# Kernel tuning notes

Measured on AMD Instinct MI355X. Metric: run time of the kernel, lower is better.

The kernel has to match this reference:

```python
import jax, jax.numpy as jnp
import numpy as np
import math

B, L, D = 2, 2048, 1024
H = 16
DH = D // H  # 64
XPOS_SCALE_BASE = 512.0
THETA = 10000.0


def setup_inputs() -> dict:
    key = jax.random.key(0)
    ks = jax.random.split(key, 9)
    s = 0.02  # keep logits in a sane range like trained weights
    return {
        "x": jax.random.normal(ks[0], (B, L, D), dtype=jnp.float32),
        "Wq": jax.random.normal(ks[1], (D, D), dtype=jnp.float32) * s,
        "bq": jax.random.normal(ks[2], (D,), dtype=jnp.float32) * s,
        "Wk": jax.random.normal(ks[3], (D, D), dtype=jnp.float32) * s,
        "bk": jax.random.normal(ks[4], (D,), dtype=jnp.float32) * s,
        "Wv": jax.random.normal(ks[5], (D, D), dtype=jnp.float32) * s,
        "bv": jax.random.normal(ks[6], (D,), dtype=jnp.float32) * s,
        "Wo": jax.random.normal(ks[7], (D, D), dtype=jnp.float32) * s,
        "bo": jax.random.normal(ks[8], (D,), dtype=jnp.float32) * s,
    }


def _rotate_half(t):
    # pairwise interleaved rotation, as in rotary_embedding_torch
    t1 = t[..., 0::2]
    t2 = t[..., 1::2]
    return jnp.stack([-t2, t1], axis=-1).reshape(t.shape)


def _xpos_rotate(q, k):
    # q, k: [B, H, L, DH]; xPos rotary embedding (use_xpos=True)
    seq = q.shape[2]
    half = jnp.arange(0, DH, 2, dtype=jnp.float32)
    inv_freq = 1.0 / (THETA ** (half / DH))            # [DH/2]
    t = jnp.arange(seq, dtype=jnp.float32)             # [L]
    freqs = t[:, None] * inv_freq[None, :]             # [L, DH/2]
    freqs = jnp.repeat(freqs, 2, axis=-1)              # [L, DH] interleaved
    # xPos length-extrapolatable scale
    scale_vec = (half + 0.4 * DH) / (1.4 * DH)         # [DH/2]
    power = (t - seq // 2) / XPOS_SCALE_BASE           # [L]
    scale = scale_vec[None, :] ** power[:, None]       # [L, DH/2]
    scale = jnp.repeat(scale, 2, axis=-1)              # [L, DH]
    cos = jnp.cos(freqs)
    sin = jnp.sin(freqs)
    q_out = q * (cos * scale) + _rotate_half(q) * (sin * scale)
    k_out = k * (cos / scale) + _rotate_half(k) * (sin / scale)
    return q_out, k_out


def reference(x, Wq, bq, Wk, bk, Wv, bv, Wo, bo):
    b, l, d = x.shape
    # projections; note source swaps names: v_mat <- k-proj, k_mat <- v-proj
    q = (x @ Wq.T + bq).reshape(b, l, H, DH).transpose(0, 2, 1, 3)  # [b,h,l,dh]
    v = (x @ Wk.T + bk).reshape(b, l, H, DH).transpose(0, 2, 1, 3)
    k = (x @ Wv.T + bv).reshape(b, l, H, DH).transpose(0, 2, 1, 3)
    q, k = _xpos_rotate(q, k)
    # source divides by sqrt(Dh * num_heads) == sqrt(dim)
    scores = jnp.einsum("bhqd,bhkd->bhqk", q, k) / math.sqrt(d)
    weights = jax.nn.softmax(scores, axis=-1)
    inter = jnp.einsum("bhqk,bhkd->bhqd", weights, v)
    inter = inter.transpose(0, 2, 1, 3).reshape(b, l, d)
    return inter @ Wo.T + bo
```

## Files before the change

kernel.cpp:

```cpp
#include <hip/hip_runtime.h>
#include <math.h>

#define NB 2
#define NL 2048
#define ND 1024
#define NH 16
#define NDH 64
#define NBL 4096

typedef __attribute__((ext_vector_type(4)))  float f32x4;
typedef __attribute__((ext_vector_type(16))) float f32x16;
typedef __attribute__((ext_vector_type(8)))  short s16x8;
typedef __attribute__((ext_vector_type(4)))  short s16x4;

#define LOG2E 1.44269504088896f

__device__ __forceinline__ float fexp2(float x){
#if __has_builtin(__builtin_amdgcn_exp2f)
  return __builtin_amdgcn_exp2f(x);
#else
  return exp2f(x);
#endif
}

__device__ __forceinline__ unsigned short f2bf(float f){
  unsigned int u = __float_as_uint(f);
  u += 0x7FFF + ((u >> 16) & 1);
  return (unsigned short)(u >> 16);
}

__device__ __forceinline__ unsigned int pk2bf(float lo, float hi){
  return __builtin_amdgcn_perm(__float_as_uint(hi) + 0x8000u,
                               __float_as_uint(lo) + 0x8000u, 0x07060302u);
}

__global__ void cvt_all(const float* __restrict__ x,
                        const float* __restrict__ wq, const float* __restrict__ wk,
                        const float* __restrict__ wv, const float* __restrict__ wo,
                        unsigned short* __restrict__ xb,
                        unsigned short* __restrict__ wqb, unsigned short* __restrict__ wkb,
                        unsigned short* __restrict__ wvb, unsigned short* __restrict__ wob,
                        float2* __restrict__ qtab, float2* __restrict__ ktab){
  int i = blockIdx.x * blockDim.x + threadIdx.x;
  if (i < (1<<21)){
    const float* s; unsigned short* d; int off;
    if (i < (1<<20)) { s = x; d = xb; off = i; }
    else {
      int j = i - (1<<20); int w = j >> 18; off = j & ((1<<18)-1);
      s = (w==0)?wq:(w==1)?wk:(w==2)?wv:wo;
      d = (w==0)?wqb:(w==1)?wkb:(w==2)?wvb:wob;
    }
    float4 f = reinterpret_cast<const float4*>(s)[off];
    ushort4 r; r.x=f2bf(f.x); r.y=f2bf(f.y); r.z=f2bf(f.z); r.w=f2bf(f.w);
    reinterpret_cast<ushort4*>(d)[off] = r;
  } else {
    int t = i - (1<<21);
    int l = t >> 5, k = t & 31;
    float half = 2.0f * (float)k;
    float inv_freq = 1.0f / powf(10000.0f, half / 64.0f);
    float fr = (float)l * inv_freq;
    float sv = (half + 0.4f * 64.0f) / (1.4f * 64.0f);
    float pw = ((float)l - 1024.0f) / 512.0f;
    float sc = powf(sv, pw);
    float cs = cosf(fr), sn = sinf(fr);
    qtab[t] = make_float2(cs * sc, sn * sc);
    ktab[t] = make_float2(cs / sc, sn / sc);
  }
}

__global__ __launch_bounds__(256, 4) void gemm_qkv(
    const unsigned short* __restrict__ A,
    const unsigned short* __restrict__ Wq, const float* __restrict__ bq,
    const unsigned short* __restrict__ Wk, const float* __restrict__ bk,
    const unsigned short* __restrict__ Wv, const float* __restrict__ bv,
    unsigned short* __restrict__ qb, unsigned short* __restrict__ kb,
    unsigned short* __restrict__ vtb,
    const float2* __restrict__ qtab, const float2* __restrict__ ktab)
{
  __shared__ unsigned short smem[9216];

  const int mode = blockIdx.z;
  const unsigned short* W = (mode==0) ? Wq : (mode==1) ? Wk : Wv;
  const float* bias       = (mode==0) ? bq : (mode==1) ? bk : bv;

  const int tid  = threadIdx.x;
  const int wave = tid >> 6, lane = tid & 63;
  const int m16  = lane & 15, quad = lane >> 4;
  const int mrow = (wave & 1) * 64, ncol = (wave >> 1) * 32;
  const int rA   = lane >> 2, cA = (lane & 3) * 8;
  const int row0 = blockIdx.x * 128, col0 = blockIdx.y * 64;

  f32x4 acc[4][2] = {};

  for (int k0 = 0; k0 < ND; k0 += 32){
    __syncthreads();
#pragma unroll
    for (int i3 = 0; i3 < 3; i3++){
      const int c = wave * 3 + i3;
      const unsigned short* g; unsigned short* l;
      if (c < 8){ g = A + (size_t)(row0 + c*16 + rA) * ND + k0 + cA;      l = &smem[c*512]; }
      else      { g = W + (size_t)(col0 + (c-8)*16 + rA) * ND + k0 + cA;  l = &smem[4096 + (c-8)*512]; }
      __builtin_amdgcn_global_load_lds((const __attribute__((address_space(1))) void*)g,
                                       (__attribute__((address_space(3))) void*)l, 16, 0, 0);
    }
    __syncthreads();
    s16x8 af[4], bf[2];
#pragma unroll
    for (int mt = 0; mt < 4; mt++)
      af[mt] = *reinterpret_cast<const s16x8*>(&smem[(mrow + mt*16 + m16)*32 + quad*8]);
#pragma unroll
    for (int nt = 0; nt < 2; nt++)
      bf[nt] = *reinterpret_cast<const s16x8*>(&smem[4096 + (ncol + nt*16 + m16)*32 + quad*8]);
#pragma unroll
    for (int mt = 0; mt < 4; mt++)
#pragma unroll
      for (int nt = 0; nt < 2; nt++)
        acc[mt][nt] = __builtin_amdgcn_mfma_f32_16x16x32_bf16(af[mt], bf[nt], acc[mt][nt], 0, 0, 0);
  }
  __syncthreads();

  const int b  = row0 >> 11, l0 = row0 & (NL - 1);
  const int h  = col0 >> 6;
  const int bh = b * NH + h;

  if (mode == 2){
#pragma unroll
    for (int mt = 0; mt < 4; mt++)
#pragma unroll
      for (int nt = 0; nt < 2; nt++)
#pragma unroll
        for (int r = 0; r < 4; r++){
          int lrow = mrow + mt*16 + quad*4 + r;
          int dhl  = ncol + nt*16 + m16;
          smem[lrow*72 + dhl] = f2bf(acc[mt][nt][r] + bias[col0 + dhl]);
        }
  } else {
    const float qscale = (mode == 0) ? (0.03125f * LOG2E) : 1.0f;
    const float2* tab  = (mode == 0) ? qtab : ktab;
#pragma unroll
    for (int mt = 0; mt < 4; mt++)
#pragma unroll
      for (int nt = 0; nt < 2; nt++)
#pragma unroll
        for (int r = 0; r < 4; r++){
          int lrow = mrow + mt*16 + quad*4 + r;
          int dhl  = ncol + nt*16 + m16;
          float v  = acc[mt][nt][r] + bias[col0 + dhl];
          float pv = __shfl_xor(v, 1);
          float2 t = tab[(l0 + lrow)*32 + (dhl >> 1)];
          float rh = (dhl & 1) ? pv : -pv;
          smem[lrow*72 + dhl] = f2bf((v * t.x + rh * t.y) * qscale);
        }
  }
  __syncthreads();

  if (mode == 2){
#pragma unroll
    for (int j4 = 0; j4 < 4; j4++){
      int c = tid * 4 + j4;
      int d = c >> 4, seg = (c & 15) * 8;
      unsigned short tmp[8];
#pragma unroll
      for (int jj = 0; jj < 8; jj++) tmp[jj] = smem[(seg + jj)*72 + d];
      *reinterpret_cast<uint4*>(vtb + (size_t)(bh * NDH + d) * NL + l0 + seg) =
          *reinterpret_cast<uint4*>(tmp);
    }
  } else {
    unsigned short* dst = ((mode == 0) ? qb : kb) + ((size_t)bh * NL + l0) * NDH;
#pragma unroll
    for (int j = 0; j < 4; j++){
      int idx = j*256 + tid;
      int row = idx >> 3, cg = (idx & 7) * 8;
      *reinterpret_cast<uint4*>(dst + row*NDH + cg) =
          *reinterpret_cast<const uint4*>(&smem[row*72 + cg]);
    }
  }
}

__global__ __launch_bounds__(256) void gemm_o(
    const unsigned short* __restrict__ A, const unsigned short* __restrict__ W,
    const float* __restrict__ bias, float* __restrict__ out)
{
  __shared__ unsigned short As[128][32];
  __shared__ unsigned short Bs[64][32];
  const int tid  = threadIdx.x;
  const int wave = tid >> 6, lane = tid & 63;
  const int m16  = lane & 15, quad = lane >> 4;
  const int mrow = (wave & 1) * 64, ncol = (wave >> 1) * 32;
  const int rA   = lane >> 2, cA = (lane & 3) * 8;
  const int row0 = blockIdx.x * 128, col0 = blockIdx.y * 64;

  f32x4 acc[4][2] = {};

  for (int k0 = 0; k0 < ND; k0 += 32){
    __syncthreads();
#pragma unroll
    for (int i3 = 0; i3 < 3; i3++){
      const int c = wave * 3 + i3;
      const unsigned short* g; unsigned short* l;
      if (c < 8){ g = A + (size_t)(row0 + c*16 + rA) * ND + k0 + cA;      l = &As[c*16][0]; }
      else      { g = W + (size_t)(col0 + (c-8)*16 + rA) * ND + k0 + cA;  l = &Bs[(c-8)*16][0]; }
      __builtin_amdgcn_global_load_lds((const __attribute__((address_space(1))) void*)g,
                                       (__attribute__((address_space(3))) void*)l, 16, 0, 0);
    }
    __syncthreads();
    s16x8 af[4], bf[2];
#pragma unroll
    for (int mt = 0; mt < 4; mt++) af[mt] = *reinterpret_cast<const s16x8*>(&As[mrow + mt*16 + m16][quad*8]);
#pragma unroll
    for (int nt = 0; nt < 2; nt++) bf[nt] = *reinterpret_cast<const s16x8*>(&Bs[ncol + nt*16 + m16][quad*8]);
#pragma unroll
    for (int mt = 0; mt < 4; mt++)
#pragma unroll
      for (int nt = 0; nt < 2; nt++)
        acc[mt][nt] = __builtin_amdgcn_mfma_f32_16x16x32_bf16(af[mt], bf[nt], acc[mt][nt], 0, 0, 0);
  }

#pragma unroll
  for (int mt = 0; mt < 4; mt++)
#pragma unroll
    for (int nt = 0; nt < 2; nt++)
#pragma unroll
      for (int r = 0; r < 4; r++){
        int grow = row0 + mrow + mt*16 + quad*4 + r;
        int gcol = col0 + ncol + nt*16 + m16;
        out[(size_t)grow * ND + gcol] = acc[mt][nt][r] + bias[gcol];
      }
}

__global__ __launch_bounds__(256, 2) void attn_kernel(
    const unsigned short* __restrict__ qb,
    const unsigned short* __restrict__ kb,
    const unsigned short* __restrict__ vtb,
    unsigned short* __restrict__ opart,
    float* __restrict__ lsum)
{
  __shared__ unsigned short smem[256 * 72];
  const int tid  = threadIdx.x;
  const int wave = tid >> 6, lane = tid & 63;
  const int l31  = lane & 31, g = lane >> 5;
  const int bh   = blockIdx.y;
  const int z    = blockIdx.z;
  const int q0   = blockIdx.x * 256;
  const int kbase = z * (NL / 2);
  const unsigned short* Q  = qb  + (size_t)bh * NL * NDH;
  const unsigned short* K  = kb  + (size_t)bh * NL * NDH;
  const unsigned short* Vt = vtb + (size_t)bh * NDH * NL;

  s16x8 qf[2][4];
#pragma unroll
  for (int q2 = 0; q2 < 2; q2++)
#pragma unroll
    for (int s = 0; s < 4; s++)
      qf[q2][s] = *reinterpret_cast<const s16x8*>(
          Q + (size_t)(q0 + wave*64 + q2*32 + l31) * NDH + s*16 + g*8);

  const int r0 = tid >> 3, c0 = tid & 7;
  const int r1 = r0 + 32;
  const int so0 = r0*64 + ((c0 ^ (r0 & 7)) * 8);
  const int so1 = r1*64 + ((c0 ^ (r1 & 7)) * 8);

  uint4 kreg0 = *reinterpret_cast<const uint4*>(K  + (size_t)(kbase + r0) * NDH + c0*8);
  uint4 kreg1 = *reinterpret_cast<const uint4*>(K  + (size_t)(kbase + r1) * NDH + c0*8);
  uint4 vreg0 = *reinterpret_cast<const uint4*>(Vt + (size_t)r0 * NL + kbase + c0*8);
  uint4 vreg1 = *reinterpret_cast<const uint4*>(Vt + (size_t)r1 * NL + kbase + c0*8);
  *reinterpret_cast<uint4*>(&smem[so0])         = kreg0;
  *reinterpret_cast<uint4*>(&smem[so1])         = kreg1;
  *reinterpret_cast<uint4*>(&smem[8192 + so0])  = vreg0;
  *reinterpret_cast<uint4*>(&smem[8192 + so1])  = vreg1;
  kreg0 = *reinterpret_cast<const uint4*>(K  + (size_t)(kbase + 64 + r0) * NDH + c0*8);
  kreg1 = *reinterpret_cast<const uint4*>(K  + (size_t)(kbase + 64 + r1) * NDH + c0*8);
  vreg0 = *reinterpret_cast<const uint4*>(Vt + (size_t)r0 * NL + kbase + 64 + c0*8);
  vreg1 = *reinterpret_cast<const uint4*>(Vt + (size_t)r1 * NL + kbase + 64 + c0*8);
  __syncthreads();

  float ls[2] = {0.f, 0.f};
  f32x16 ot[2][2] = {};
  const int key7 = l31 & 7;

  for (int kt = 0; kt < 16; kt++){
    const int cur = (kt & 1) * 4096;
    const int nxt = 4096 - cur;
    if (kt < 15){
      *reinterpret_cast<uint4*>(&smem[nxt + so0])        = kreg0;
      *reinterpret_cast<uint4*>(&smem[nxt + so1])        = kreg1;
      *reinterpret_cast<uint4*>(&smem[8192 + nxt + so0]) = vreg0;
      *reinterpret_cast<uint4*>(&smem[8192 + nxt + so1]) = vreg1;
    }
    if (kt < 14){
      const int k0n = kbase + (kt + 2) * 64;
      kreg0 = *reinterpret_cast<const uint4*>(K  + (size_t)(k0n + r0) * NDH + c0*8);
      kreg1 = *reinterpret_cast<const uint4*>(K  + (size_t)(k0n + r1) * NDH + c0*8);
      vreg0 = *reinterpret_cast<const uint4*>(Vt + (size_t)r0 * NL + k0n + c0*8);
      vreg1 = *reinterpret_cast<const uint4*>(Vt + (size_t)r1 * NL + k0n + c0*8);
    }

    const unsigned short* Kb = &smem[cur];
    const unsigned short* Vb = &smem[8192 + cur];

    uint2 pmat[2][8];
#pragma unroll
    for (int t = 0; t < 2; t++){
      f32x16 st0 = {}, st1 = {};
#pragma unroll
      for (int s = 0; s < 4; s++){
        const int cg = (2*s + g) ^ key7;
        s16x8 kf = *reinterpret_cast<const s16x8*>(&Kb[(t*32 + l31)*64 + cg*8]);
        st0 = __builtin_amdgcn_mfma_f32_32x32x16_bf16(kf, qf[0][s], st0, 0, 0, 0);
        st1 = __builtin_amdgcn_mfma_f32_32x32x16_bf16(kf, qf[1][s], st1, 0, 0, 0);
      }
#pragma unroll
      for (int j = 0; j < 4; j++){
        float a0 = fexp2(st0[4*j]), a1 = fexp2(st0[4*j+1]);
        float a2 = fexp2(st0[4*j+2]), a3 = fexp2(st0[4*j+3]);
        ls[0] += (a0 + a1) + (a2 + a3);
        pmat[0][t*4+j].x = pk2bf(a0, a1);
        pmat[0][t*4+j].y = pk2bf(a2, a3);
        float b0 = fexp2(st1[4*j]), b1 = fexp2(st1[4*j+1]);
        float b2 = fexp2(st1[4*j+2]), b3 = fexp2(st1[4*j+3]);
        ls[1] += (b0 + b1) + (b2 + b3);
        pmat[1][t*4+j].x = pk2bf(b0, b1);
        pmat[1][t*4+j].y = pk2bf(b2, b3);
      }
    }

#pragma unroll
    for (int mt = 0; mt < 2; mt++){
      const int dh = mt*32 + l31;
#pragma unroll
      for (int s = 0; s < 8; s++){
        const int cg = s ^ (dh & 7);
        s16x4 vf = *reinterpret_cast<const s16x4*>(&Vb[dh*64 + cg*8 + g*4]);
        ot[mt][0] = __builtin_amdgcn_mfma_f32_32x32x8bf16_1k(
            vf, *reinterpret_cast<s16x4*>(&pmat[0][s]), ot[mt][0], 0, 0, 0);
        ot[mt][1] = __builtin_amdgcn_mfma_f32_32x32x8bf16_1k(
            vf, *reinterpret_cast<s16x4*>(&pmat[1][s]), ot[mt][1], 0, 0, 0);
      }
    }
    __syncthreads();
  }

#pragma unroll
  for (int q2 = 0; q2 < 2; q2++){
    float t = ls[q2] + __shfl_xor(ls[q2], 32);
    if (g == 0)
      lsum[((size_t)z * NB * NH + bh) * NL + q0 + wave*64 + q2*32 + l31] = t;
  }

#pragma unroll
  for (int mt = 0; mt < 2; mt++)
#pragma unroll
    for (int q2 = 0; q2 < 2; q2++)
#pragma unroll
      for (int s = 0; s < 4; s++){
        uint2 pk;
        pk.x = pk2bf(ot[mt][q2][4*s], ot[mt][q2][4*s + 1]);
        pk.y = pk2bf(ot[mt][q2][4*s + 2], ot[mt][q2][4*s + 3]);
        *reinterpret_cast<uint2*>(&smem[(wave*64 + q2*32 + l31)*72 + mt*32 + s*8 + g*4]) = pk;
      }
  __syncthreads();

  const int bb = bh >> 4, h = bh & 15;
  unsigned short* od = opart + (size_t)z * NBL * ND;
#pragma unroll
  for (int j = 0; j < 8; j++){
    int idx = j*256 + tid;
    int row = idx >> 3, cg2 = (idx & 7) * 8;
    *reinterpret_cast<uint4*>(od + ((size_t)(bb*NL + q0 + row)) * ND + h*NDH + cg2) =
        *reinterpret_cast<const uint4*>(&smem[row*72 + cg2]);
  }
}

__device__ __forceinline__ unsigned int comb2(unsigned int a, unsigned int b, float inv){
  float alo = __uint_as_float(a << 16), ahi = __uint_as_float(a & 0xFFFF0000u);
  float blo = __uint_as_float(b << 16), bhi = __uint_as_float(b & 0xFFFF0000u);
  return pk2bf((alo + blo) * inv, (ahi + bhi) * inv);
}

__global__ __launch_bounds__(256) void attn_combine(
    unsigned short* __restrict__ opart, const float* __restrict__ lsum)
{
  int idx = blockIdx.x * 256 + threadIdx.x;
  int row = idx >> 7;
  int col8 = idx & 127;
  int h = col8 >> 3;
  int b = row >> 11, l = row & (NL - 1);
  int bh = b * NH + h;
  float l0 = lsum[(size_t)bh * NL + l];
  float l1 = lsum[(size_t)(NB*NH + bh) * NL + l];
  float inv = 1.0f / (l0 + l1);
  uint4 u0 = reinterpret_cast<const uint4*>(opart)[idx];
  uint4 u1 = reinterpret_cast<const uint4*>(opart + (size_t)NBL * ND)[idx];
  uint4 o;
  o.x = comb2(u0.x, u1.x, inv);
  o.y = comb2(u0.y, u1.y, inv);
  o.z = comb2(u0.z, u1.z, inv);
  o.w = comb2(u0.w, u1.w, inv);
  reinterpret_cast<uint4*>(opart)[idx] = o;
}

extern "C" void kernel_launch(void* const* d_in, const int* in_sizes, int n_in,
                              void* d_out, int out_size, void* d_ws, size_t ws_size,
                              hipStream_t stream)
{
  (void)in_sizes; (void)n_in; (void)out_size; (void)ws_size;
  const float* x  = (const float*)d_in[0];
  const float* Wq = (const float*)d_in[1];
  const float* bq = (const float*)d_in[2];
  const float* Wk = (const float*)d_in[3];
  const float* bk = (const float*)d_in[4];
  const float* Wv = (const float*)d_in[5];
  const float* bv = (const float*)d_in[6];
  const float* Wo = (const float*)d_in[7];
  const float* bo = (const float*)d_in[8];
  float* out = (float*)d_out;

  char* p = (char*)d_ws;
  unsigned short* xb    = (unsigned short*)p; p += (size_t)NBL*ND*2;
  unsigned short* wqb   = (unsigned short*)p; p += (size_t)ND*ND*2;
  unsigned short* wkb   = (unsigned short*)p; p += (size_t)ND*ND*2;
  unsigned short* wvb   = (unsigned short*)p; p += (size_t)ND*ND*2;
  unsigned short* wob   = (unsigned short*)p; p += (size_t)ND*ND*2;
  unsigned short* qbuf  = (unsigned short*)p; p += (size_t)NBL*ND*2;
  unsigned short* kbuf  = (unsigned short*)p; p += (size_t)NBL*ND*2;
  unsigned short* vtb   = (unsigned short*)p; p += (size_t)NBL*ND*2;
  unsigned short* opart = (unsigned short*)p; p += (size_t)2*NBL*ND*2;
  float* lsum = (float*)p; p += (size_t)2*NB*NH*NL*4;
  float2* qtab = (float2*)p; p += (size_t)NL*32*8;
  float2* ktab = (float2*)p; p += (size_t)NL*32*8;

  hipLaunchKernelGGL(cvt_all, dim3(8448), dim3(256), 0, stream,
                     x, Wq, Wk, Wv, Wo, xb, wqb, wkb, wvb, wob, qtab, ktab);

  hipLaunchKernelGGL(gemm_qkv, dim3(NBL/128, ND/64, 3), dim3(256), 0, stream,
                     xb, wqb, bq, wvb, bv, wkb, bk, qbuf, kbuf, vtb, qtab, ktab);

  hipLaunchKernelGGL(attn_kernel, dim3(NL/256, NB*NH, 2), dim3(256), 0, stream,
                     qbuf, kbuf, vtb, opart, lsum);
  hipLaunchKernelGGL(attn_combine, dim3(NBL*ND/8/256), dim3(256), 0, stream, opart, lsum);

  hipLaunchKernelGGL(gemm_o, dim3(NBL/128, ND/64), dim3(256), 0, stream, opart, wob, bo, out);
}
```

Baseline: 208.1 us.

## Widen QKV GEMM tile to 128x128 with per-head two-pass epilogue

Doubles the N dimension of the QKV projection tile from 64 to 128 columns, so each wave computes a 64x64 subtile with 4x4 MFMA accumulators and each k-step loads A and B tiles evenly. This halves the grid and raises arithmetic intensity per loaded A tile, cutting global/LDS traffic for the activation matrix. The epilogue is split into two passes, one per head, reusing the shared staging buffer with extra barriers. Register pressure rises, so the launch bound is lowered from 4 to 3 blocks per CU, and the smaller grid (768 blocks) may reduce load balance.

Measured after the change: 199.8 us. -4.0%, faster.

```diff
diff --git a/kernel.cpp b/kernel.cpp
--- a/kernel.cpp
+++ b/kernel.cpp
@@ -68,7 +68,7 @@
   }
 }
 
-__global__ __launch_bounds__(256, 4) void gemm_qkv(
+__global__ __launch_bounds__(256, 3) void gemm_qkv(
     const unsigned short* __restrict__ A,
     const unsigned short* __restrict__ Wq, const float* __restrict__ bq,
     const unsigned short* __restrict__ Wk, const float* __restrict__ bk,
@@ -86,94 +86,100 @@
   const int tid  = threadIdx.x;
   const int wave = tid >> 6, lane = tid & 63;
   const int m16  = lane & 15, quad = lane >> 4;
-  const int mrow = (wave & 1) * 64, ncol = (wave >> 1) * 32;
+  const int mrow = (wave & 1) * 64, ncol = (wave >> 1) * 64;
   const int rA   = lane >> 2, cA = (lane & 3) * 8;
-  const int row0 = blockIdx.x * 128, col0 = blockIdx.y * 64;
-
-  f32x4 acc[4][2] = {};
+  const int row0 = blockIdx.x * 128, col0 = blockIdx.y * 128;
+
+  f32x4 acc[4][4] = {};
 
   for (int k0 = 0; k0 < ND; k0 += 32){
     __syncthreads();
 #pragma unroll
-    for (int i3 = 0; i3 < 3; i3++){
-      const int c = wave * 3 + i3;
-      const unsigned short* g; unsigned short* l;
-      if (c < 8){ g = A + (size_t)(row0 + c*16 + rA) * ND + k0 + cA;      l = &smem[c*512]; }
-      else      { g = W + (size_t)(col0 + (c-8)*16 + rA) * ND + k0 + cA;  l = &smem[4096 + (c-8)*512]; }
-      __builtin_amdgcn_global_load_lds((const __attribute__((address_space(1))) void*)g,
-                                       (__attribute__((address_space(3))) void*)l, 16, 0, 0);
-    }
-    __syncthreads();
-    s16x8 af[4], bf[2];
+    for (int i2 = 0; i2 < 2; i2++){
+      const int c = wave * 2 + i2;
+      const unsigned short* ga = A + (size_t)(row0 + c*16 + rA) * ND + k0 + cA;
+      const unsigned short* gb = W + (size_t)(col0 + c*16 + rA) * ND + k0 + cA;
+      __builtin_amdgcn_global_load_lds((const __attribute__((address_space(1))) void*)ga,
+                                       (__attribute__((address_space(3))) void*)&smem[c*512], 16, 0, 0);
+      __builtin_amdgcn_global_load_lds((const __attribute__((address_space(1))) void*)gb,
+                                       (__attribute__((address_space(3))) void*)&smem[4096 + c*512], 16, 0, 0);
+    }
+    __syncthreads();
+    s16x8 af[4], bf[4];
 #pragma unroll
     for (int mt = 0; mt < 4; mt++)
       af[mt] = *reinterpret_cast<const s16x8*>(&smem[(mrow + mt*16 + m16)*32 + quad*8]);
 #pragma unroll
-    for (int nt = 0; nt < 2; nt++)
+    for (int nt = 0; nt < 4; nt++)
       bf[nt] = *reinterpret_cast<const s16x8*>(&smem[4096 + (ncol + nt*16 + m16)*32 + quad*8]);
 #pragma unroll
     for (int mt = 0; mt < 4; mt++)
 #pragma unroll
-      for (int nt = 0; nt < 2; nt++)
+      for (int nt = 0; nt < 4; nt++)
         acc[mt][nt] = __builtin_amdgcn_mfma_f32_16x16x32_bf16(af[mt], bf[nt], acc[mt][nt], 0, 0, 0);
   }
   __syncthreads();
 
   const int b  = row0 >> 11, l0 = row0 & (NL - 1);
-  const int h  = col0 >> 6;
-  const int bh = b * NH + h;
-
-  if (mode == 2){
-#pragma unroll
-    for (int mt = 0; mt < 4; mt++)
-#pragma unroll
-      for (int nt = 0; nt < 2; nt++)
-#pragma unroll
-        for (int r = 0; r < 4; r++){
-          int lrow = mrow + mt*16 + quad*4 + r;
-          int dhl  = ncol + nt*16 + m16;
-          smem[lrow*72 + dhl] = f2bf(acc[mt][nt][r] + bias[col0 + dhl]);
-        }
-  } else {
-    const float qscale = (mode == 0) ? (0.03125f * LOG2E) : 1.0f;
-    const float2* tab  = (mode == 0) ? qtab : ktab;
-#pragma unroll
-    for (int mt = 0; mt < 4; mt++)
-#pragma unroll
-      for (int nt = 0; nt < 2; nt++)
-#pragma unroll
-        for (int r = 0; r < 4; r++){
-          int lrow = mrow + mt*16 + quad*4 + r;
-          int dhl  = ncol + nt*16 + m16;
-          float v  = acc[mt][nt][r] + bias[col0 + dhl];
-          float pv = __shfl_xor(v, 1);
-          float2 t = tab[(l0 + lrow)*32 + (dhl >> 1)];
-          float rh = (dhl & 1) ? pv : -pv;
-          smem[lrow*72 + dhl] = f2bf((v * t.x + rh * t.y) * qscale);
-        }
-  }
-  __syncthreads();
-
-  if (mode == 2){
-#pragma unroll
-    for (int j4 = 0; j4 < 4; j4++){
-      int c = tid * 4 + j4;
-      int d = c >> 4, seg = (c & 15) * 8;
-      unsigned short tmp[8];
-#pragma unroll
-      for (int jj = 0; jj < 8; jj++) tmp[jj] = smem[(seg + jj)*72 + d];
-      *reinterpret_cast<uint4*>(vtb + (size_t)(bh * NDH + d) * NL + l0 + seg) =
-          *reinterpret_cast<uint4*>(tmp);
-    }
-  } else {
-    unsigned short* dst = ((mode == 0) ? qb : kb) + ((size_t)bh * NL + l0) * NDH;
-#pragma unroll
-    for (int j = 0; j < 4; j++){
-      int idx = j*256 + tid;
-      int row = idx >> 3, cg = (idx & 7) * 8;
-      *reinterpret_cast<uint4*>(dst + row*NDH + cg) =
-          *reinterpret_cast<const uint4*>(&smem[row*72 + cg]);
-    }
+
+#pragma unroll
+  for (int h2 = 0; h2 < 2; h2++){
+    if ((wave >> 1) == h2){
+      if (mode == 2){
+#pragma unroll
+        for (int mt = 0; mt < 4; mt++)
+#pragma unroll
+          for (int nt = 0; nt < 4; nt++)
+#pragma unroll
+            for (int r = 0; r < 4; r++){
+              int lrow = mrow + mt*16 + quad*4 + r;
+              int dh   = nt*16 + m16;
+              smem[lrow*72 + dh] = f2bf(acc[mt][nt][r] + bias[col0 + h2*64 + dh]);
+            }
+      } else {
+        const float qscale = (mode == 0) ? (0.03125f * LOG2E) : 1.0f;
+        const float2* tab  = (mode == 0) ? qtab : ktab;
+#pragma unroll
+        for (int mt = 0; mt < 4; mt++)
+#pragma unroll
+          for (int nt = 0; nt < 4; nt++)
+#pragma unroll
+            for (int r = 0; r < 4; r++){
+              int lrow = mrow + mt*16 + quad*4 + r;
+              int dh   = nt*16 + m16;
+              float v  = acc[mt][nt][r] + bias[col0 + h2*64 + dh];
+              float pv = __shfl_xor(v, 1);
+              float2 t = tab[(l0 + lrow)*32 + (dh >> 1)];
+              float rh = (dh & 1) ? pv : -pv;
+              smem[lrow*72 + dh] = f2bf((v * t.x + rh * t.y) * qscale);
+            }
+      }
+    }
+    __syncthreads();
+
+    const int bh = b * NH + (col0 >> 6) + h2;
+    if (mode == 2){
+#pragma unroll
+      for (int j4 = 0; j4 < 4; j4++){
+        int c = tid * 4 + j4;
+        int d = c >> 4, seg = (c & 15) * 8;
+        unsigned short tmp[8];
+#pragma unroll
+        for (int jj = 0; jj < 8; jj++) tmp[jj] = smem[(seg + jj)*72 + d];
+        *reinterpret_cast<uint4*>(vtb + (size_t)(bh * NDH + d) * NL + l0 + seg) =
+            *reinterpret_cast<uint4*>(tmp);
+      }
+    } else {
+      unsigned short* dst = ((mode == 0) ? qb : kb) + ((size_t)bh * NL + l0) * NDH;
+#pragma unroll
+      for (int j = 0; j < 4; j++){
+        int idx = j*256 + tid;
+        int row = idx >> 3, cg = (idx & 7) * 8;
+        *reinterpret_cast<uint4*>(dst + row*NDH + cg) =
+            *reinterpret_cast<const uint4*>(&smem[row*72 + cg]);
+      }
+    }
+    __syncthreads();
   }
 }
 
@@ -311,12 +317,12 @@
       }
 #pragma unroll
       for (int j = 0; j < 4; j++){
-        float a0 = fexp2(st0[4*j]), a1 = fexp2(st0[4*j+1]);
+        float a0 = fexp2(st0[4*j]),   a1 = fexp2(st0[4*j+1]);
         float a2 = fexp2(st0[4*j+2]), a3 = fexp2(st0[4*j+3]);
         ls[0] += (a0 + a1) + (a2 + a3);
         pmat[0][t*4+j].x = pk2bf(a0, a1);
         pmat[0][t*4+j].y = pk2bf(a2, a3);
-        float b0 = fexp2(st1[4*j]), b1 = fexp2(st1[4*j+1]);
+        float b0 = fexp2(st1[4*j]),   b1 = fexp2(st1[4*j+1]);
         float b2 = fexp2(st1[4*j+2]), b3 = fexp2(st1[4*j+3]);
         ls[1] += (b0 + b1) + (b2 + b3);
         pmat[1][t*4+j].x = pk2bf(b0, b1);
@@ -354,7 +360,7 @@
 #pragma unroll
       for (int s = 0; s < 4; s++){
         uint2 pk;
-        pk.x = pk2bf(ot[mt][q2][4*s], ot[mt][q2][4*s + 1]);
+        pk.x = pk2bf(ot[mt][q2][4*s],     ot[mt][q2][4*s + 1]);
         pk.y = pk2bf(ot[mt][q2][4*s + 2], ot[mt][q2][4*s + 3]);
         *reinterpret_cast<uint2*>(&smem[(wave*64 + q2*32 + l31)*72 + mt*32 + s*8 + g*4]) = pk;
       }
@@ -432,7 +438,7 @@
   hipLaunchKernelGGL(cvt_all, dim3(8448), dim3(256), 0, stream,
                      x, Wq, Wk, Wv, Wo, xb, wqb, wkb, wvb, wob, qtab, ktab);
 
-  hipLaunchKernelGGL(gemm_qkv, dim3(NBL/128, ND/64, 3), dim3(256), 0, stream,
+  hipLaunchKernelGGL(gemm_qkv, dim3(NBL/128, ND/128, 3), dim3(256), 0, stream,
                      xb, wqb, bq, wvb, bv, wkb, bk, qbuf, kbuf, vtb, qtab, ktab);
 
   hipLaunchKernelGGL(attn_kernel, dim3(NL/256, NB*NH, 2), dim3(256), 0, stream,
```
